# Optimization experiments

Measured on AMD Instinct MI355X. Metric: run time of the kernel, lower is better.

The kernel has to match this reference:

```python
import jax, jax.numpy as jnp
import numpy as np

N, G, E, H, Z = 50000, 2000, 800000, 512, 64
BN_EPS = 1e-5


def setup_inputs() -> dict:
    key = jax.random.key(0)
    ks = jax.random.split(key, 10)
    x = jax.random.normal(ks[0], (N, G), dtype=jnp.float32)
    edge_index = jax.random.randint(ks[1], (2, E), 0, N, dtype=jnp.int32)
    s1 = 1.0 / np.sqrt(G)
    s2 = 1.0 / np.sqrt(H)
    return {
        "x": x,
        "edge_index": edge_index,
        "W1l": jax.random.normal(ks[2], (G, H), dtype=jnp.float32) * s1,
        "b1": jnp.zeros((H,), jnp.float32),
        "W1r": jax.random.normal(ks[3], (G, H), dtype=jnp.float32) * s1,
        "bn_gamma": jax.random.uniform(ks[4], (H,), dtype=jnp.float32) + 0.5,
        "bn_beta": jax.random.normal(ks[5], (H,), dtype=jnp.float32) * 0.1,
        "bn_mean": jax.random.normal(ks[6], (H,), dtype=jnp.float32) * 0.1,
        "bn_var": jax.random.uniform(ks[7], (H,), dtype=jnp.float32) + 0.5,
        "W2l": jax.random.normal(ks[8], (H, Z), dtype=jnp.float32) * s2,
        "b2": jnp.zeros((Z,), jnp.float32),
        "W2r": jax.random.normal(ks[9], (H, Z), dtype=jnp.float32) * s2,
    }


def _sage_conv(h, src, dst, Wl, bl, Wr, n_nodes):
    # mean aggregation of source features at destination nodes
    msg = h[src]  # [E, D] gather
    agg = jax.ops.segment_sum(msg, dst, num_segments=n_nodes)
    cnt = jax.ops.segment_sum(jnp.ones((src.shape[0],), h.dtype), dst, num_segments=n_nodes)
    agg = agg / jnp.maximum(cnt, 1.0)[:, None]
    # PyG SAGEConv: lin_l(agg) + lin_r(x), bias only on lin_l
    return agg @ Wl + bl + h @ Wr


def reference(x, edge_index, W1l, b1, W1r, bn_gamma, bn_beta, bn_mean, bn_var, W2l, b2, W2r):
    src, dst = edge_index[0], edge_index[1]
    n = x.shape[0]
    h = _sage_conv(x, src, dst, W1l, b1, W1r, n)  # [N, H]
    # BatchNorm1d (eval mode: running stats) + ReLU; dropout is identity at inference
    h = (h - bn_mean) * (bn_gamma / jnp.sqrt(bn_var + BN_EPS)) + bn_beta
    h = jax.nn.relu(h)
    z = _sage_conv(h, src, dst, W2l, b2, W2r, n)  # [N, Z]
    return z
```

## Files before the change

kernel.cpp:

```cpp
#include <hip/hip_runtime.h>


#define BN_EPS 1e-5f
#define GK 2000
#define KP 2048
#define NT1 64
#define NT2 16

typedef __attribute__((ext_vector_type(8))) short bf16x8;
typedef __attribute__((ext_vector_type(4))) float f32x4;
typedef unsigned short u16x8 __attribute__((ext_vector_type(8)));

__device__ inline unsigned short f2bf(float f) {
    union { float f; unsigned u; } v; v.f = f;
    unsigned r = (v.u + 0x7fffu + ((v.u >> 16) & 1u)) >> 16;
    return (unsigned short)r;
}
__device__ inline float bf2f(unsigned short u) {
    union { unsigned u; float f; } v; v.u = ((unsigned)u) << 16;
    return v.f;
}

#define GLL16(gp, lp) __builtin_amdgcn_global_load_lds( \
    (const __attribute__((address_space(1))) void*)(gp), \
    (__attribute__((address_space(3))) void*)(lp), 16, 0, 0)

__global__ __launch_bounds__(256) void prep_fused(
    const float* __restrict__ W1l, const float* __restrict__ W1r,
    const float* __restrict__ gamma, const float* __restrict__ beta,
    const float* __restrict__ mean, const float* __restrict__ var,
    const float* __restrict__ b1, unsigned short* __restrict__ BT,
    const float* __restrict__ W2l, const float* __restrict__ W2r,
    unsigned short* __restrict__ BT2, float* __restrict__ b1p,
    const int* __restrict__ ei, int* __restrict__ cnt, int E)
{
    const int bb = blockIdx.x;
    if (bb < 1024) {
        int idx = bb * 256 + threadIdx.x;
        int c  = idx >> 8;
        int k0 = (idx & 255) << 3;
        int cc = (c < 512) ? c : c - 512;
        float scv = gamma[cc] * rsqrtf(var[cc] + BN_EPS);
        const float* W = (c < 512) ? (W1l + cc) : (W1r + cc);
        unsigned short us[8];
#pragma unroll
        for (int j = 0; j < 8; ++j) {
            int k = k0 + j;
            float v = (k < GK) ? W[(size_t)k * 512] * scv : 0.0f;
            us[j] = f2bf(v);
        }
        *(u16x8*)&BT[(size_t)c * KP + k0] = *(u16x8*)us;
    } else if (bb < 1056) {
        int idx = (bb - 1024) * 256 + threadIdx.x;
        int c  = idx >> 6;
        int k0 = (idx & 63) << 3;
        const float* W = (c < 64) ? (W2l + c) : (W2r + (c - 64));
        unsigned short us[8];
#pragma unroll
        for (int j = 0; j < 8; ++j) us[j] = f2bf(W[(size_t)(k0 + j) * 64]);
        *(u16x8*)&BT2[(size_t)c * 512 + k0] = *(u16x8*)us;
    } else if (bb == 1056) {
#pragma unroll
        for (int h = 0; h < 2; ++h) {
            int c = threadIdx.x + h * 256;
            float scv = gamma[c] * rsqrtf(var[c] + BN_EPS);
            b1p[c] = b1[c] * scv + (beta[c] - mean[c] * scv);
        }
    } else {
        for (int i = (bb - 1057) * 256 + threadIdx.x; i < E; i += 1024 * 256)
            atomicAdd(&cnt[ei[E + i]], 1);
    }
}

__global__ __launch_bounds__(1024) void scan_kernel(const int* __restrict__ cnt,
                                                    int* __restrict__ row_start, int n) {
    __shared__ int part[1024];
    int t = threadIdx.x;
    int chunk = (n + 1023) >> 10;
    int lo = t * chunk;
    int hi = lo + chunk; if (hi > n) hi = n;
    int s = 0;
    for (int i = lo; i < hi; ++i) s += cnt[i];
    part[t] = s;
    __syncthreads();
    for (int off = 1; off < 1024; off <<= 1) {
        int add = (t >= off) ? part[t - off] : 0;
        __syncthreads();
        part[t] += add;
        __syncthreads();
    }
    int run = (t == 0) ? 0 : part[t - 1];
    for (int i = lo; i < hi; ++i) { row_start[i] = run; run += cnt[i]; }
    if (t == 1023) row_start[n] = part[1023];
}

__global__ __launch_bounds__(256) void convfill_kernel(
    const float* __restrict__ x, unsigned short* __restrict__ xb, int N,
    const int* __restrict__ ei, int E, const int* __restrict__ row_start,
    int* __restrict__ cnt, int* __restrict__ colidx)
{
    const int bb = blockIdx.x;
    if (bb < 2048) {
        const int total8 = N * 256;
        for (int idx = bb * 256 + threadIdx.x; idx < total8; idx += 2048 * 256) {
            int row = idx >> 8;
            int k8  = idx & 255;
            unsigned short us[8];
            if (k8 < 250) {
                const float4* p = (const float4*)(x + (size_t)row * 2000 + k8 * 8);
                float4 v0 = p[0], v1 = p[1];
                us[0]=f2bf(v0.x); us[1]=f2bf(v0.y); us[2]=f2bf(v0.z); us[3]=f2bf(v0.w);
                us[4]=f2bf(v1.x); us[5]=f2bf(v1.y); us[6]=f2bf(v1.z); us[7]=f2bf(v1.w);
            } else {
#pragma unroll
                for (int j = 0; j < 8; ++j) us[j] = 0;
            }
            *(u16x8*)&xb[(size_t)row * 2048 + k8 * 8] = *(u16x8*)us;
        }
    } else {
        int i = (bb - 2048) * 256 + threadIdx.x;
        if (i < E) {
            int d = ei[E + i];
            int p = atomicSub(&cnt[d], 1) - 1;
            colidx[row_start[d] + p] = ei[i];
        }
    }
}

__global__ __launch_bounds__(512) void gemm1_256(
    const unsigned short* __restrict__ xb, int M,
    const unsigned short* __restrict__ BT,
    unsigned short* __restrict__ Y)
{
    __shared__ __align__(16) unsigned short As[3][8192];
    __shared__ __align__(16) unsigned short Bs[3][8192];

    const int t = threadIdx.x, wid = t >> 6, lane = t & 63;
    const int nbr = (M + 255) >> 8;
    const int nwg = nbr * 4;
    const int b   = blockIdx.x;
    int swz;
    if ((nwg & 7) == 0) swz = (b & 7) * (nwg >> 3) + (b >> 3);
    else swz = b;
    const int row0 = (swz >> 2) << 8;
    const int col0 = (swz & 3) << 8;

    const int c0 = t, c1 = t + 512;
    const int g0 = ((c0 & 3) ^ ((c0 >> 3) & 3)) << 3;
    const int g1 = ((c1 & 3) ^ ((c1 >> 3) & 3)) << 3;
    int ra0 = row0 + (c0 >> 2); if (ra0 >= M) ra0 = M - 1;
    int ra1 = row0 + (c1 >> 2); if (ra1 >= M) ra1 = M - 1;
    const unsigned short* aS0 = xb + (size_t)ra0 * KP + g0;
    const unsigned short* aS1 = xb + (size_t)ra1 * KP + g1;
    const unsigned short* bS0 = BT + (size_t)(col0 + (c0 >> 2)) * KP + g0;
    const unsigned short* bS1 = BT + (size_t)(col0 + (c1 >> 2)) * KP + g1;

    const int wr = wid >> 2, wc = wid & 3;
    const int fr16 = lane & 15;
    const int gswr = ((lane >> 4) ^ ((fr16 >> 1) & 3)) << 4;

    f32x4 acc[8][4];
#pragma unroll
    for (int m = 0; m < 8; ++m)
#pragma unroll
        for (int n = 0; n < 4; ++n) acc[m][n] = (f32x4)0.0f;

#define STG(kt, buf) do {                                          \
        unsigned short* ab_ = &As[buf][0];                         \
        unsigned short* bb_ = &Bs[buf][0];                         \
        GLL16(aS0 + (size_t)(kt) * 32, ab_ + c0 * 8);              \
        GLL16(aS1 + (size_t)(kt) * 32, ab_ + c1 * 8);              \
        GLL16(bS0 + (size_t)(kt) * 32, bb_ + c0 * 8);              \
        GLL16(bS1 + (size_t)(kt) * 32, bb_ + c1 * 8);              \
    } while (0)

    STG(0, 0);
    STG(1, 1);

    int rb = 0;
    for (int it = 0; it < NT1; ++it) {
        if (it == NT1 - 1) {
            asm volatile("s_waitcnt vmcnt(0)" ::: "memory");
        } else {
            asm volatile("s_waitcnt vmcnt(4)" ::: "memory");
        }
        __builtin_amdgcn_s_barrier();
        __builtin_amdgcn_sched_barrier(0);

        const char* Ab = (const char*)&As[rb][0];
        const char* Bb = (const char*)&Bs[rb][0];
        bf16x8 af[8], bfr[4];
#pragma unroll
        for (int m = 0; m < 8; ++m)
            af[m] = *(const bf16x8*)(Ab + ((wr * 128 + m * 16 + fr16) << 6) + gswr);
#pragma unroll
        for (int n = 0; n < 4; ++n)
            bfr[n] = *(const bf16x8*)(Bb + ((wc * 64 + n * 16 + fr16) << 6) + gswr);

        if (it + 2 < NT1) {
            int wb = rb + 2; if (wb >= 3) wb -= 3;
            STG(it + 2, wb);
        }

        __builtin_amdgcn_s_setprio(1);
#pragma unroll
        for (int m = 0; m < 8; ++m)
#pragma unroll
            for (int n = 0; n < 4; ++n)
                acc[m][n] = __builtin_amdgcn_mfma_f32_16x16x32_bf16(
                    af[m], bfr[n], acc[m][n], 0, 0, 0);
        __builtin_amdgcn_s_setprio(0);

        rb = (rb == 2) ? 0 : rb + 1;
    }
#undef STG

    const int crow = (lane >> 4) << 2;
#pragma unroll
    for (int m = 0; m < 8; ++m) {
        int rbase = row0 + wr * 128 + m * 16 + crow;
#pragma unroll
        for (int r = 0; r < 4; ++r) {
            int row = rbase + r;
            if (row < M) {
                unsigned short* Yp = Y + (size_t)row * 1024 + col0 + wc * 64 + fr16;
#pragma unroll
                for (int n = 0; n < 4; ++n)
                    Yp[n * 16] = f2bf(acc[m][n][r]);
            }
        }
    }
}

__global__ __launch_bounds__(256) void agg1_kernel(
    const unsigned short* __restrict__ Y, unsigned short* __restrict__ Hh,
    const int* __restrict__ row_start, const int* __restrict__ colidx,
    const float* __restrict__ b1p, int n)
{
    int wid  = (blockIdx.x * blockDim.x + threadIdx.x) >> 6;
    int lane = threadIdx.x & 63;
    if (wid >= n) return;
    int c0 = lane * 8;
    float bb[8];
    *(float4*)&bb[0] = *(const float4*)&b1p[c0];
    *(float4*)&bb[4] = *(const float4*)&b1p[c0 + 4];

    int s0 = row_start[wid], s1 = row_start[wid + 1];
    float acc[8] = {0, 0, 0, 0, 0, 0, 0, 0};
    int i = s0;
    for (; i + 2 <= s1; i += 2) {
        int src0 = colidx[i], src1 = colidx[i + 1];
        u16x8 v0 = *(const u16x8*)&Y[(size_t)src0 * 1024 + c0];
        u16x8 v1 = *(const u16x8*)&Y[(size_t)src1 * 1024 + c0];
#pragma unroll
        for (int j = 0; j < 8; ++j) acc[j] += bf2f(v0[j]) + bf2f(v1[j]);
    }
    if (i < s1) {
        int src = colidx[i];
        u16x8 v = *(const u16x8*)&Y[(size_t)src * 1024 + c0];
#pragma unroll
        for (int j = 0; j < 8; ++j) acc[j] += bf2f(v[j]);
    }
    float inv = 1.0f / fmaxf((float)(s1 - s0), 1.0f);
    u16x8 sv = *(const u16x8*)&Y[(size_t)wid * 1024 + 512 + c0];
    unsigned short o[8];
#pragma unroll
    for (int j = 0; j < 8; ++j) {
        float pre = acc[j] * inv + bb[j] + bf2f(sv[j]);
        o[j] = f2bf(fmaxf(pre, 0.0f));
    }
    *(u16x8*)&Hh[(size_t)wid * 512 + c0] = *(u16x8*)o;
}

__global__ __launch_bounds__(256) void gemm2_bf16(
    const unsigned short* __restrict__ Hh, int M,
    const unsigned short* __restrict__ BT2,
    unsigned short* __restrict__ U)
{
    __shared__ __align__(16) unsigned short As[2][128][32];
    __shared__ __align__(16) unsigned short Bs[2][128][32];

    const int t    = threadIdx.x;
    const int wid  = t >> 6;
    const int lane = t & 63;
    const int row0 = blockIdx.x << 7;

    const int c_lo = wid * 64 + lane;
    const int c_hi = c_lo + 256;
    const int s_lo = ((c_lo & 3) ^ ((c_lo >> 3) & 3)) << 3;
    const int s_hi = ((c_hi & 3) ^ ((c_hi >> 3) & 3)) << 3;
    int ra = row0 + (c_lo >> 2); if (ra >= M) ra = M - 1;
    int rbw = row0 + (c_hi >> 2); if (rbw >= M) rbw = M - 1;
    const unsigned short* aSrc0 = Hh + (size_t)ra * 512 + s_lo;
    const unsigned short* aSrc1 = Hh + (size_t)rbw * 512 + s_hi;
    const unsigned short* bSrc0 = BT2 + (size_t)(c_lo >> 2) * 512 + s_lo;
    const unsigned short* bSrc1 = BT2 + (size_t)(c_hi >> 2) * 512 + s_hi;

    const int wr   = wid >> 1, wc = wid & 1;
    const int fr16 = lane & 15;
    const int gsw2 = ((lane >> 4) ^ ((fr16 >> 1) & 3)) << 4;

    f32x4 acc[4][4];
#pragma unroll
    for (int m = 0; m < 4; ++m)
#pragma unroll
        for (int n = 0; n < 4; ++n) acc[m][n] = (f32x4)0.0f;

#define STAGE2(kt, buf) do {                                                  \
        int ko = (kt) * 32;                                                   \
        GLL16(aSrc0 + ko, (unsigned short*)&As[buf][0][0] + (size_t)c_lo * 8);  \
        GLL16(aSrc1 + ko, (unsigned short*)&As[buf][0][0] + (size_t)c_hi * 8);  \
        GLL16(bSrc0 + ko, (unsigned short*)&Bs[buf][0][0] + (size_t)c_lo * 8);  \
        GLL16(bSrc1 + ko, (unsigned short*)&Bs[buf][0][0] + (size_t)c_hi * 8);  \
    } while (0)

    STAGE2(0, 0);
    int cur = 0;
    for (int it = 0; it < NT2; ++it) {
        __syncthreads();
        if (it + 1 < NT2) STAGE2(it + 1, cur ^ 1);

        const char* Ab = (const char*)&As[cur][0][0];
        const char* Bb = (const char*)&Bs[cur][0][0];
        bf16x8 af[4], bfr[4];
#pragma unroll
        for (int m = 0; m < 4; ++m)
            af[m] = *(const bf16x8*)(Ab + ((wr * 64 + m * 16 + fr16) << 6) + gsw2);
#pragma unroll
        for (int n = 0; n < 4; ++n)
            bfr[n] = *(const bf16x8*)(Bb + ((wc * 64 + n * 16 + fr16) << 6) + gsw2);
#pragma unroll
        for (int m = 0; m < 4; ++m)
#pragma unroll
            for (int n = 0; n < 4; ++n)
                acc[m][n] = __builtin_amdgcn_mfma_f32_16x16x32_bf16(
                    af[m], bfr[n], acc[m][n], 0, 0, 0);
        cur ^= 1;
    }
#undef STAGE2

    const int crow = (lane >> 4) << 2;
#pragma unroll
    for (int m = 0; m < 4; ++m) {
        int rbase = row0 + wr * 64 + m * 16 + crow;
#pragma unroll
        for (int r = 0; r < 4; ++r) {
            int row = rbase + r;
            if (row < M) {
                unsigned short* Up = U + (size_t)row * 128 + wc * 64 + fr16;
#pragma unroll
                for (int n = 0; n < 4; ++n)
                    Up[n * 16] = f2bf(acc[m][n][r]);
            }
        }
    }
}

__global__ __launch_bounds__(256) void agg2_kernel(
    const unsigned short* __restrict__ U,
    const int* __restrict__ row_start, const int* __restrict__ colidx,
    const float* __restrict__ b2, float* __restrict__ out, int n)
{
    int wid  = (blockIdx.x * blockDim.x + threadIdx.x) >> 6;
    int lane = threadIdx.x & 63;
    if (wid >= n) return;
    int s0 = row_start[wid], s1 = row_start[wid + 1];
    float acc = 0.f;
    int i = s0;
    for (; i + 2 <= s1; i += 2) {
        int src0 = colidx[i], src1 = colidx[i + 1];
        acc += bf2f(U[(size_t)src0 * 128 + lane]) + bf2f(U[(size_t)src1 * 128 + lane]);
    }
    if (i < s1) acc += bf2f(U[(size_t)colidx[i] * 128 + lane]);
    float inv = 1.0f / fmaxf((float)(s1 - s0), 1.0f);
    float z = acc * inv + b2[lane] + bf2f(U[(size_t)wid * 128 + 64 + lane]);
    out[(size_t)wid * 64 + lane] = z;
}

extern "C" void kernel_launch(void* const* d_in, const int* in_sizes, int n_in,
                              void* d_out, int out_size, void* d_ws, size_t ws_size,
                              hipStream_t stream) {
    const float* x     = (const float*)d_in[0];
    const int*   ei    = (const int*)d_in[1];
    const float* W1l   = (const float*)d_in[2];
    const float* b1    = (const float*)d_in[3];
    const float* W1r   = (const float*)d_in[4];
    const float* gamma = (const float*)d_in[5];
    const float* beta  = (const float*)d_in[6];
    const float* mean  = (const float*)d_in[7];
    const float* var   = (const float*)d_in[8];
    const float* W2l   = (const float*)d_in[9];
    const float* b2    = (const float*)d_in[10];
    const float* W2r   = (const float*)d_in[11];
    float* out = (float*)d_out;

    const int N = in_sizes[0] / 2000;
    const int E = in_sizes[1] / 2;
    const int nby = (N + 127) / 128;

    char* ws = (char*)d_ws;
    unsigned short* xb  = (unsigned short*)ws;
    unsigned short* Y   = xb + (size_t)N * KP;
    unsigned short* BT  = Y + (size_t)N * 1024;
    unsigned short* BT2 = BT + (size_t)1024 * KP;
    float* b1p     = (float*)(BT2 + (size_t)128 * 512);
    int* cnt       = (int*)(b1p + 512);
    int* row_start = cnt + N;
    int* colidx    = row_start + N + 4;
    unsigned short* Hh = xb;
    unsigned short* U  = Y;

    hipMemsetAsync(cnt, 0, (size_t)N * sizeof(int), stream);

    prep_fused<<<2081, 256, 0, stream>>>(
        W1l, W1r, gamma, beta, mean, var, b1, BT, W2l, W2r, BT2, b1p,
        ei, cnt, E);

    scan_kernel<<<1, 1024, 0, stream>>>(cnt, row_start, N);

    int eb = (E + 255) / 256;
    convfill_kernel<<<2048 + eb, 256, 0, stream>>>(
        x, xb, N, ei, E, row_start, cnt, colidx);

    int nbr = (N + 255) / 256;
    gemm1_256<<<nbr * 4, 512, 0, stream>>>(xb, N, BT, Y);
    agg1_kernel<<<(N + 3) / 4, 256, 0, stream>>>(
        Y, Hh, row_start, colidx, b1p, N);
    gemm2_bf16<<<nby, 256, 0, stream>>>(Hh, N, BT2, U);
    agg2_kernel<<<(N + 3) / 4, 256, 0, stream>>>(
        U, row_start, colidx, b2, out, N);
}
```

Measured before the change: 694.1 us.

## Restructure gemm1 into K=64 double-buffered tiles with four-phase interleaved schedule

The first-layer GEMM now uses K-tiles of 64 instead of 32, with two LDS buffers instead of three, and an 8-way XOR swizzle. Each K-iteration is split into four MFMA quadrants (A-half by B-half). Barriers, LDS fragment loads and half-tile global-to-LDS prefetches are interleaved between the quadrants so memory traffic overlaps with matrix math, in the style of a ping-pong schedule. The aim is fewer barriers per unit of K and better hiding of load latency. The cost is more barriers within each iteration and a fragile vmcnt/lgkmcnt accounting, including prefetches issued past the final tile (tk+2 up to 33).

```diff
diff --git a/kernel.cpp b/kernel.cpp
--- a/kernel.cpp
+++ b/kernel.cpp
@@ -4,7 +4,7 @@
 #define BN_EPS 1e-5f
 #define GK 2000
 #define KP 2048
-#define NT1 64
+#define NKT 32
 #define NT2 16
 
 typedef __attribute__((ext_vector_type(8))) short bf16x8;
@@ -132,32 +132,49 @@
     const unsigned short* __restrict__ BT,
     unsigned short* __restrict__ Y)
 {
-    __shared__ __align__(16) unsigned short As[3][8192];
-    __shared__ __align__(16) unsigned short Bs[3][8192];
+    __shared__ __align__(16) unsigned short As[2][16384];
+    __shared__ __align__(16) unsigned short Bs[2][16384];
 
     const int t = threadIdx.x, wid = t >> 6, lane = t & 63;
     const int nbr = (M + 255) >> 8;
     const int nwg = nbr * 4;
     const int b   = blockIdx.x;
-    int swz;
-    if ((nwg & 7) == 0) swz = (b & 7) * (nwg >> 3) + (b >> 3);
-    else swz = b;
+    int swz = ((nwg & 7) == 0) ? (b & 7) * (nwg >> 3) + (b >> 3) : b;
     const int row0 = (swz >> 2) << 8;
     const int col0 = (swz & 3) << 8;
 
-    const int c0 = t, c1 = t + 512;
-    const int g0 = ((c0 & 3) ^ ((c0 >> 3) & 3)) << 3;
-    const int g1 = ((c1 & 3) ^ ((c1 >> 3) & 3)) << 3;
-    int ra0 = row0 + (c0 >> 2); if (ra0 >= M) ra0 = M - 1;
-    int ra1 = row0 + (c1 >> 2); if (ra1 >= M) ra1 = M - 1;
-    const unsigned short* aS0 = xb + (size_t)ra0 * KP + g0;
-    const unsigned short* aS1 = xb + (size_t)ra1 * KP + g1;
-    const unsigned short* bS0 = BT + (size_t)(col0 + (c0 >> 2)) * KP + g0;
-    const unsigned short* bS1 = BT + (size_t)(col0 + (c1 >> 2)) * KP + g1;
+    const unsigned short* aSrc[4];
+    const unsigned short* bSrc[4];
+#pragma unroll
+    for (int j = 0; j < 4; ++j) {
+        int c = t + 512 * j;
+        int l = (c & 7) ^ ((c >> 3) & 7);
+        int rA = row0 + (c >> 3); if (rA >= M) rA = M - 1;
+        aSrc[j] = xb + (size_t)rA * KP + l * 8;
+        bSrc[j] = BT + (size_t)(col0 + (c >> 3)) * KP + l * 8;
+    }
+
+#define STG_HA0(kt, buf) do { \
+        GLL16(aSrc[0] + (size_t)(kt) * 64, &As[buf][(size_t)t * 8]); \
+        GLL16(aSrc[1] + (size_t)(kt) * 64, &As[buf][(size_t)(t + 512) * 8]); } while (0)
+#define STG_HA1(kt, buf) do { \
+        GLL16(aSrc[2] + (size_t)(kt) * 64, &As[buf][(size_t)(1024 + t) * 8]); \
+        GLL16(aSrc[3] + (size_t)(kt) * 64, &As[buf][(size_t)(1536 + t) * 8]); } while (0)
+#define STG_HB0(kt, buf) do { \
+        GLL16(bSrc[0] + (size_t)(kt) * 64, &Bs[buf][(size_t)t * 8]); \
+        GLL16(bSrc[1] + (size_t)(kt) * 64, &Bs[buf][(size_t)(t + 512) * 8]); } while (0)
+#define STG_HB1(kt, buf) do { \
+        GLL16(bSrc[2] + (size_t)(kt) * 64, &Bs[buf][(size_t)(1024 + t) * 8]); \
+        GLL16(bSrc[3] + (size_t)(kt) * 64, &Bs[buf][(size_t)(1536 + t) * 8]); } while (0)
 
     const int wr = wid >> 2, wc = wid & 3;
     const int fr16 = lane & 15;
-    const int gswr = ((lane >> 4) ^ ((fr16 >> 1) & 3)) << 4;
+    const int j4  = lane >> 4;
+    const int sl7 = fr16 & 7;
+    const int sA0 = ((j4    ) ^ sl7) << 4;
+    const int sA1 = ((4 + j4) ^ sl7) << 4;
+    const int rbA = (wr * 128 + fr16) << 7;
+    const int rbB = (wc * 64  + fr16) << 7;
 
     f32x4 acc[8][4];
 #pragma unroll
@@ -165,55 +182,105 @@
 #pragma unroll
         for (int n = 0; n < 4; ++n) acc[m][n] = (f32x4)0.0f;
 
-#define STG(kt, buf) do {                                          \
-        unsigned short* ab_ = &As[buf][0];                         \
-        unsigned short* bb_ = &Bs[buf][0];                         \
-        GLL16(aS0 + (size_t)(kt) * 32, ab_ + c0 * 8);              \
-        GLL16(aS1 + (size_t)(kt) * 32, ab_ + c1 * 8);              \
-        GLL16(bS0 + (size_t)(kt) * 32, bb_ + c0 * 8);              \
-        GLL16(bS1 + (size_t)(kt) * 32, bb_ + c1 * 8);              \
-    } while (0)
-
-    STG(0, 0);
-    STG(1, 1);
-
-    int rb = 0;
-    for (int it = 0; it < NT1; ++it) {
-        if (it == NT1 - 1) {
-            asm volatile("s_waitcnt vmcnt(0)" ::: "memory");
-        } else {
-            asm volatile("s_waitcnt vmcnt(4)" ::: "memory");
-        }
+    STG_HB0(0, 0); STG_HA0(0, 0); STG_HA1(0, 0); STG_HB1(0, 0);
+    STG_HB0(1, 1); STG_HA0(1, 1); STG_HA1(1, 1);
+    asm volatile("s_waitcnt vmcnt(6)" ::: "memory");
+    __builtin_amdgcn_s_barrier();
+    __builtin_amdgcn_sched_barrier(0);
+
+    for (int tk = 0; tk < NKT; ++tk) {
+        const int buf = tk & 1, obuf = buf ^ 1;
+        const char* Ab = (const char*)&As[buf][0];
+        const char* Bb = (const char*)&Bs[buf][0];
+        bf16x8 af[4][2], bfA[2][2], bfB[2][2];
+
+#pragma unroll
+        for (int m = 0; m < 4; ++m) {
+            af[m][0] = *(const bf16x8*)(Ab + rbA + (m << 11) + sA0);
+            af[m][1] = *(const bf16x8*)(Ab + rbA + (m << 11) + sA1);
+        }
+#pragma unroll
+        for (int n = 0; n < 2; ++n) {
+            bfA[n][0] = *(const bf16x8*)(Bb + rbB + (n << 11) + sA0);
+            bfA[n][1] = *(const bf16x8*)(Bb + rbB + (n << 11) + sA1);
+        }
+        STG_HB1(tk + 1, obuf);
         __builtin_amdgcn_s_barrier();
         __builtin_amdgcn_sched_barrier(0);
-
-        const char* Ab = (const char*)&As[rb][0];
-        const char* Bb = (const char*)&Bs[rb][0];
-        bf16x8 af[8], bfr[4];
-#pragma unroll
-        for (int m = 0; m < 8; ++m)
-            af[m] = *(const bf16x8*)(Ab + ((wr * 128 + m * 16 + fr16) << 6) + gswr);
-#pragma unroll
-        for (int n = 0; n < 4; ++n)
-            bfr[n] = *(const bf16x8*)(Bb + ((wc * 64 + n * 16 + fr16) << 6) + gswr);
-
-        if (it + 2 < NT1) {
-            int wb = rb + 2; if (wb >= 3) wb -= 3;
-            STG(it + 2, wb);
-        }
-
         __builtin_amdgcn_s_setprio(1);
 #pragma unroll
-        for (int m = 0; m < 8; ++m)
-#pragma unroll
-            for (int n = 0; n < 4; ++n)
+        for (int m = 0; m < 4; ++m)
+#pragma unroll
+            for (int n = 0; n < 2; ++n) {
                 acc[m][n] = __builtin_amdgcn_mfma_f32_16x16x32_bf16(
-                    af[m], bfr[n], acc[m][n], 0, 0, 0);
+                    af[m][0], bfA[n][0], acc[m][n], 0, 0, 0);
+                acc[m][n] = __builtin_amdgcn_mfma_f32_16x16x32_bf16(
+                    af[m][1], bfA[n][1], acc[m][n], 0, 0, 0);
+            }
         __builtin_amdgcn_s_setprio(0);
 
-        rb = (rb == 2) ? 0 : rb + 1;
-    }
-#undef STG
+#pragma unroll
+        for (int n = 0; n < 2; ++n) {
+            bfB[n][0] = *(const bf16x8*)(Bb + rbB + ((n + 2) << 11) + sA0);
+            bfB[n][1] = *(const bf16x8*)(Bb + rbB + ((n + 2) << 11) + sA1);
+        }
+        asm volatile("s_waitcnt lgkmcnt(0)" ::: "memory");
+        __builtin_amdgcn_s_barrier();
+        __builtin_amdgcn_sched_barrier(0);
+        __builtin_amdgcn_s_setprio(1);
+#pragma unroll
+        for (int m = 0; m < 4; ++m)
+#pragma unroll
+            for (int n = 0; n < 2; ++n) {
+                acc[m][n + 2] = __builtin_amdgcn_mfma_f32_16x16x32_bf16(
+                    af[m][0], bfB[n][0], acc[m][n + 2], 0, 0, 0);
+                acc[m][n + 2] = __builtin_amdgcn_mfma_f32_16x16x32_bf16(
+                    af[m][1], bfB[n][1], acc[m][n + 2], 0, 0, 0);
+            }
+        __builtin_amdgcn_s_setprio(0);
+
+#pragma unroll
+        for (int m = 0; m < 4; ++m) {
+            af[m][0] = *(const bf16x8*)(Ab + rbA + ((m + 4) << 11) + sA0);
+            af[m][1] = *(const bf16x8*)(Ab + rbA + ((m + 4) << 11) + sA1);
+        }
+        STG_HB0(tk + 2, buf);
+        asm volatile("s_waitcnt lgkmcnt(0)" ::: "memory");
+        __builtin_amdgcn_s_barrier();
+        __builtin_amdgcn_sched_barrier(0);
+        __builtin_amdgcn_s_setprio(1);
+#pragma unroll
+        for (int m = 0; m < 4; ++m)
+#pragma unroll
+            for (int n = 0; n < 2; ++n) {
+                acc[m + 4][n] = __builtin_amdgcn_mfma_f32_16x16x32_bf16(
+                    af[m][0], bfA[n][0], acc[m + 4][n], 0, 0, 0);
+                acc[m + 4][n] = __builtin_amdgcn_mfma_f32_16x16x32_bf16(
+                    af[m][1], bfA[n][1], acc[m + 4][n], 0, 0, 0);
+            }
+        __builtin_amdgcn_s_setprio(0);
+
+        STG_HA0(tk + 2, buf);
+        STG_HA1(tk + 2, buf);
+        asm volatile("s_waitcnt vmcnt(6)" ::: "memory");
+        __builtin_amdgcn_s_barrier();
+        __builtin_amdgcn_sched_barrier(0);
+        __builtin_amdgcn_s_setprio(1);
+#pragma unroll
+        for (int m = 0; m < 4; ++m)
+#pragma unroll
+            for (int n = 0; n < 2; ++n) {
+                acc[m + 4][n + 2] = __builtin_amdgcn_mfma_f32_16x16x32_bf16(
+                    af[m][0], bfB[n][0], acc[m + 4][n + 2], 0, 0, 0);
+                acc[m + 4][n + 2] = __builtin_amdgcn_mfma_f32_16x16x32_bf16(
+                    af[m][1], bfB[n][1], acc[m + 4][n + 2], 0, 0, 0);
+            }
+        __builtin_amdgcn_s_setprio(0);
+    }
+#undef STG_HA0
+#undef STG_HA1
+#undef STG_HB0
+#undef STG_HB1
 
     const int crow = (lane >> 4) << 2;
 #pragma unroll
@@ -277,8 +344,8 @@
     const unsigned short* __restrict__ BT2,
     unsigned short* __restrict__ U)
 {
-    __shared__ __align__(16) unsigned short As[2][128][32];
-    __shared__ __align__(16) unsigned short Bs[2][128][32];
+    __shared__ __align__(16) unsigned short As2[2][128][32];
+    __shared__ __align__(16) unsigned short Bs2[2][128][32];
 
     const int t    = threadIdx.x;
     const int wid  = t >> 6;
@@ -308,10 +375,10 @@
 
 #define STAGE2(kt, buf) do {                                                  \
         int ko = (kt) * 32;                                                   \
-        GLL16(aSrc0 + ko, (unsigned short*)&As[buf][0][0] + (size_t)c_lo * 8);  \
-        GLL16(aSrc1 + ko, (unsigned short*)&As[buf][0][0] + (size_t)c_hi * 8);  \
-        GLL16(bSrc0 + ko, (unsigned short*)&Bs[buf][0][0] + (size_t)c_lo * 8);  \
-        GLL16(bSrc1 + ko, (unsigned short*)&Bs[buf][0][0] + (size_t)c_hi * 8);  \
+        GLL16(aSrc0 + ko, (unsigned short*)&As2[buf][0][0] + (size_t)c_lo * 8);  \
+        GLL16(aSrc1 + ko, (unsigned short*)&As2[buf][0][0] + (size_t)c_hi * 8);  \
+        GLL16(bSrc0 + ko, (unsigned short*)&Bs2[buf][0][0] + (size_t)c_lo * 8);  \
+        GLL16(bSrc1 + ko, (unsigned short*)&Bs2[buf][0][0] + (size_t)c_hi * 8);  \
     } while (0)
 
     STAGE2(0, 0);
@@ -320,8 +387,8 @@
         __syncthreads();
         if (it + 1 < NT2) STAGE2(it + 1, cur ^ 1);
 
-        const char* Ab = (const char*)&As[cur][0][0];
-        const char* Bb = (const char*)&Bs[cur][0][0];
+        const char* Ab = (const char*)&As2[cur][0][0];
+        const char* Bb = (const char*)&Bs2[cur][0][0];
         bf16x8 af[4], bfr[4];
 #pragma unroll
         for (int m = 0; m < 4; ++m)
```

New measurement: 689.6 us. Within noise of the previous version (-0.6%).

## Fuse x conversion into prep kernel and CSR fill into gemm1 launch

Applied to the files above, without the earlier changes.

Moves the fp32-to-bf16 conversion of x into the prep kernel alongside the weight transposes and degree counting, and folds the CSR colidx fill into extra trailing blocks of the gemm1 launch. This removes one kernel launch and lets the scatter fill overlap with the GEMM tail. gemm1 also drops from a triple-buffered vmcnt-pipelined LDS scheme to a double-buffered __syncthreads scheme with launch_bounds(512,4), which cuts LDS use to allow more resident blocks but gives up the deeper prefetch. The fill blocks run after the GEMM tiles in launch order, so they may mostly trail the GEMM.

```diff
diff --git a/kernel.cpp b/kernel.cpp
--- a/kernel.cpp
+++ b/kernel.cpp
@@ -25,7 +25,8 @@
     (const __attribute__((address_space(1))) void*)(gp), \
     (__attribute__((address_space(3))) void*)(lp), 16, 0, 0)
 
-__global__ __launch_bounds__(256) void prep_fused(
+__global__ __launch_bounds__(256) void prep2(
+    const float* __restrict__ x, unsigned short* __restrict__ xb, int N,
     const float* __restrict__ W1l, const float* __restrict__ W1r,
     const float* __restrict__ gamma, const float* __restrict__ beta,
     const float* __restrict__ mean, const float* __restrict__ var,
@@ -35,8 +36,25 @@
     const int* __restrict__ ei, int* __restrict__ cnt, int E)
 {
     const int bb = blockIdx.x;
-    if (bb < 1024) {
-        int idx = bb * 256 + threadIdx.x;
+    if (bb < 2048) {
+        const int total8 = N * 256;
+        for (int idx = bb * 256 + threadIdx.x; idx < total8; idx += 2048 * 256) {
+            int row = idx >> 8;
+            int k8  = idx & 255;
+            unsigned short us[8];
+            if (k8 < 250) {
+                const float4* p = (const float4*)(x + (size_t)row * 2000 + k8 * 8);
+                float4 v0 = p[0], v1 = p[1];
+                us[0]=f2bf(v0.x); us[1]=f2bf(v0.y); us[2]=f2bf(v0.z); us[3]=f2bf(v0.w);
+                us[4]=f2bf(v1.x); us[5]=f2bf(v1.y); us[6]=f2bf(v1.z); us[7]=f2bf(v1.w);
+            } else {
+#pragma unroll
+                for (int j = 0; j < 8; ++j) us[j] = 0;
+            }
+            *(u16x8*)&xb[(size_t)row * 2048 + k8 * 8] = *(u16x8*)us;
+        }
+    } else if (bb < 3072) {
+        int idx = (bb - 2048) * 256 + threadIdx.x;
         int c  = idx >> 8;
         int k0 = (idx & 255) << 3;
         int cc = (c < 512) ? c : c - 512;
@@ -50,8 +68,8 @@
             us[j] = f2bf(v);
         }
         *(u16x8*)&BT[(size_t)c * KP + k0] = *(u16x8*)us;
-    } else if (bb < 1056) {
-        int idx = (bb - 1024) * 256 + threadIdx.x;
+    } else if (bb < 3104) {
+        int idx = (bb - 3072) * 256 + threadIdx.x;
         int c  = idx >> 6;
         int k0 = (idx & 63) << 3;
         const float* W = (c < 64) ? (W2l + c) : (W2r + (c - 64));
@@ -59,7 +77,7 @@
 #pragma unroll
         for (int j = 0; j < 8; ++j) us[j] = f2bf(W[(size_t)(k0 + j) * 64]);
         *(u16x8*)&BT2[(size_t)c * 512 + k0] = *(u16x8*)us;
-    } else if (bb == 1056) {
+    } else if (bb == 3104) {
 #pragma unroll
         for (int h = 0; h < 2; ++h) {
             int c = threadIdx.x + h * 256;
@@ -67,7 +85,7 @@
             b1p[c] = b1[c] * scv + (beta[c] - mean[c] * scv);
         }
     } else {
-        for (int i = (bb - 1057) * 256 + threadIdx.x; i < E; i += 1024 * 256)
+        for (int i = (bb - 3105) * 256 + threadIdx.x; i < E; i += 1024 * 256)
             atomicAdd(&cnt[ei[E + i]], 1);
     }
 }
@@ -94,54 +112,33 @@
     if (t == 1023) row_start[n] = part[1023];
 }
 
-__global__ __launch_bounds__(256) void convfill_kernel(
-    const float* __restrict__ x, unsigned short* __restrict__ xb, int N,
+__global__ __launch_bounds__(512, 4) void gemm1_256(
+    const unsigned short* __restrict__ xb, int M,
+    const unsigned short* __restrict__ BT,
+    unsigned short* __restrict__ Y,
     const int* __restrict__ ei, int E, const int* __restrict__ row_start,
     int* __restrict__ cnt, int* __restrict__ colidx)
 {
-    const int bb = blockIdx.x;
-    if (bb < 2048) {
-        const int total8 = N * 256;
-        for (int idx = bb * 256 + threadIdx.x; idx < total8; idx += 2048 * 256) {
-            int row = idx >> 8;
-            int k8  = idx & 255;
-            unsigned short us[8];
-            if (k8 < 250) {
-                const float4* p = (const float4*)(x + (size_t)row * 2000 + k8 * 8);
-                float4 v0 = p[0], v1 = p[1];
-                us[0]=f2bf(v0.x); us[1]=f2bf(v0.y); us[2]=f2bf(v0.z); us[3]=f2bf(v0.w);
-                us[4]=f2bf(v1.x); us[5]=f2bf(v1.y); us[6]=f2bf(v1.z); us[7]=f2bf(v1.w);
-            } else {
-#pragma unroll
-                for (int j = 0; j < 8; ++j) us[j] = 0;
-            }
-            *(u16x8*)&xb[(size_t)row * 2048 + k8 * 8] = *(u16x8*)us;
-        }
-    } else {
-        int i = (bb - 2048) * 256 + threadIdx.x;
+    __shared__ __align__(16) unsigned short As[2][8192];
+    __shared__ __align__(16) unsigned short Bs[2][8192];
+
+    const int t = threadIdx.x;
+    const int nbr = (M + 255) >> 8;
+    const int nwg = nbr * 4;
+    const int b   = blockIdx.x;
+
+    if (b >= nwg) {
+        int i = (b - nwg) * 512 + t;
         if (i < E) {
             int d = ei[E + i];
             int p = atomicSub(&cnt[d], 1) - 1;
             colidx[row_start[d] + p] = ei[i];
         }
-    }
-}
-
-__global__ __launch_bounds__(512) void gemm1_256(
-    const unsigned short* __restrict__ xb, int M,
-    const unsigned short* __restrict__ BT,
-    unsigned short* __restrict__ Y)
-{
-    __shared__ __align__(16) unsigned short As[3][8192];
-    __shared__ __align__(16) unsigned short Bs[3][8192];
-
-    const int t = threadIdx.x, wid = t >> 6, lane = t & 63;
-    const int nbr = (M + 255) >> 8;
-    const int nwg = nbr * 4;
-    const int b   = blockIdx.x;
-    int swz;
-    if ((nwg & 7) == 0) swz = (b & 7) * (nwg >> 3) + (b >> 3);
-    else swz = b;
+        return;
+    }
+
+    const int wid = t >> 6, lane = t & 63;
+    int swz = ((nwg & 7) == 0) ? (b & 7) * (nwg >> 3) + (b >> 3) : b;
     const int row0 = (swz >> 2) << 8;
     const int col0 = (swz & 3) << 8;
 
@@ -175,20 +172,13 @@
     } while (0)
 
     STG(0, 0);
-    STG(1, 1);
-
-    int rb = 0;
+    int cur = 0;
     for (int it = 0; it < NT1; ++it) {
-        if (it == NT1 - 1) {
-            asm volatile("s_waitcnt vmcnt(0)" ::: "memory");
-        } else {
-            asm volatile("s_waitcnt vmcnt(4)" ::: "memory");
-        }
-        __builtin_amdgcn_s_barrier();
-        __builtin_amdgcn_sched_barrier(0);
-
-        const char* Ab = (const char*)&As[rb][0];
-        const char* Bb = (const char*)&Bs[rb][0];
+        __syncthreads();
+        if (it + 1 < NT1) STG(it + 1, cur ^ 1);
+
+        const char* Ab = (const char*)&As[cur][0];
+        const char* Bb = (const char*)&Bs[cur][0];
         bf16x8 af[8], bfr[4];
 #pragma unroll
         for (int m = 0; m < 8; ++m)
@@ -196,11 +186,6 @@
 #pragma unroll
         for (int n = 0; n < 4; ++n)
             bfr[n] = *(const bf16x8*)(Bb + ((wc * 64 + n * 16 + fr16) << 6) + gswr);
-
-        if (it + 2 < NT1) {
-            int wb = rb + 2; if (wb >= 3) wb -= 3;
-            STG(it + 2, wb);
-        }
 
         __builtin_amdgcn_s_setprio(1);
 #pragma unroll
@@ -211,7 +196,7 @@
                     af[m], bfr[n], acc[m][n], 0, 0, 0);
         __builtin_amdgcn_s_setprio(0);
 
-        rb = (rb == 2) ? 0 : rb + 1;
+        cur ^= 1;
     }
 #undef STG
 
@@ -277,8 +262,8 @@
     const unsigned short* __restrict__ BT2,
     unsigned short* __restrict__ U)
 {
-    __shared__ __align__(16) unsigned short As[2][128][32];
-    __shared__ __align__(16) unsigned short Bs[2][128][32];
+    __shared__ __align__(16) unsigned short As2[2][128][32];
+    __shared__ __align__(16) unsigned short Bs2[2][128][32];
 
     const int t    = threadIdx.x;
     const int wid  = t >> 6;
@@ -308,10 +293,10 @@
 
 #define STAGE2(kt, buf) do {                                                  \
         int ko = (kt) * 32;                                                   \
-        GLL16(aSrc0 + ko, (unsigned short*)&As[buf][0][0] + (size_t)c_lo * 8);  \
-        GLL16(aSrc1 + ko, (unsigned short*)&As[buf][0][0] + (size_t)c_hi * 8);  \
-        GLL16(bSrc0 + ko, (unsigned short*)&Bs[buf][0][0] + (size_t)c_lo * 8);  \
-        GLL16(bSrc1 + ko, (unsigned short*)&Bs[buf][0][0] + (size_t)c_hi * 8);  \
+        GLL16(aSrc0 + ko, (unsigned short*)&As2[buf][0][0] + (size_t)c_lo * 8);  \
+        GLL16(aSrc1 + ko, (unsigned short*)&As2[buf][0][0] + (size_t)c_hi * 8);  \
+        GLL16(bSrc0 + ko, (unsigned short*)&Bs2[buf][0][0] + (size_t)c_lo * 8);  \
+        GLL16(bSrc1 + ko, (unsigned short*)&Bs2[buf][0][0] + (size_t)c_hi * 8);  \
     } while (0)
 
     STAGE2(0, 0);
@@ -320,8 +305,8 @@
         __syncthreads();
         if (it + 1 < NT2) STAGE2(it + 1, cur ^ 1);
 
-        const char* Ab = (const char*)&As[cur][0][0];
-        const char* Bb = (const char*)&Bs[cur][0][0];
+        const char* Ab = (const char*)&As2[cur][0][0];
+        const char* Bb = (const char*)&Bs2[cur][0][0];
         bf16x8 af[4], bfr[4];
 #pragma unroll
         for (int m = 0; m < 4; ++m)
@@ -412,18 +397,18 @@
 
     hipMemsetAsync(cnt, 0, (size_t)N * sizeof(int), stream);
 
-    prep_fused<<<2081, 256, 0, stream>>>(
-        W1l, W1r, gamma, beta, mean, var, b1, BT, W2l, W2r, BT2, b1p,
-        ei, cnt, E);
+    prep2<<<4129, 256, 0, stream>>>(
+        x, xb, N, W1l, W1r, gamma, beta, mean, var, b1, BT,
+        W2l, W2r, BT2, b1p, ei, cnt, E);
 
     scan_kernel<<<1, 1024, 0, stream>>>(cnt, row_start, N);
 
-    int eb = (E + 255) / 256;
-    convfill_kernel<<<2048 + eb, 256, 0, stream>>>(
-        x, xb, N, ei, E, row_start, cnt, colidx);
-
     int nbr = (N + 255) / 256;
-    gemm1_256<<<nbr * 4, 512, 0, stream>>>(xb, N, BT, Y);
+    int nwg = nbr * 4;
+    int fillb = (E + 511) / 512;
+    gemm1_256<<<nwg + fillb, 512, 0, stream>>>(
+        xb, N, BT, Y, ei, E, row_start, cnt, colidx);
+
     agg1_kernel<<<(N + 3) / 4, 256, 0, stream>>>(
         Y, Hh, row_start, colidx, b1p, N);
     gemm2_bf16<<<nby, 256, 0, stream>>>(Hh, N, BT2, U);
```

Result: slower. 2.468 ms (+255.6%).
